# Optimization experiments

Hardware: AMD Instinct MI355X
Metric: run time of the kernel (lower is better)

The kernel has to match this reference:

```python
import jax, jax.numpy as jnp
import numpy as np

B, U, P = 32, 64, 8          # dialogues, utterances per dialogue, parties per dialogue
V, D, L = 32000, 300, 256    # vocab, emb_dim, sentence length
H, S = 5, 5                  # n_heads, n_steps
NP = 200                     # global number of parties
MAXLEN = 252
NT = B * (U + P)             # total nodes in batched graph


def setup_inputs() -> dict:
    key = jax.random.key(0)
    ks = iter(jax.random.split(key, 48))
    rn = lambda shape, s=0.02: jax.random.normal(next(ks), shape, jnp.float32) * s
    x = jax.random.randint(next(ks), (B * U, L), 0, V, dtype=jnp.int32)
    ps_local = np.array(jax.random.randint(next(ks), (B, U), 0, P, dtype=jnp.int32))
    # build batched dialogue graph (sequential utterance chain + utterance<->party edges)
    src, dst = [], []
    for g in range(B):
        off = g * (U + P)
        for i in range(U - 1):
            src += [off + i, off + i + 1]; dst += [off + i + 1, off + i]
        for i in range(U):
            q = off + U + int(ps_local[g, i])
            src += [off + i, q]; dst += [q, off + i]
    src = jnp.asarray(np.array(src, np.int32)); dst = jnp.asarray(np.array(dst, np.int32))
    node_ids = np.arange(NT).reshape(B, U + P)
    u_idx = jnp.asarray(node_ids[:, :U].reshape(-1).astype(np.int32))
    q_idx = jnp.asarray(node_ids[:, U:].reshape(-1).astype(np.int32))
    lid = jnp.tile(jnp.arange(U, dtype=jnp.int32), B)
    pids = jax.random.randint(next(ks), (B * P,), 0, NP, dtype=jnp.int32)
    py = jax.random.normal(next(ks), (B,), jnp.float32)
    return dict(
        x=x, src=src, dst=dst, u_idx=u_idx, q_idx=q_idx, lid=lid, pids=pids, py=py,
        word_W=rn((V, D), 1.0),
        conv_w3=rn((100, 1, 3, D)), conv_b3=rn((100,)),
        conv_w4=rn((100, 1, 4, D)), conv_b4=rn((100,)),
        conv_w5=rn((100, 1, 5, D)), conv_b5=rn((100,)),
        party_W=rn((NP, D), 1.0), pos_W=rn((MAXLEN, D)),
        gat_fc=rn((S, D, H * D)), gat_al=rn((S, H, D)), gat_ar=rn((S, H, D)),
        gat_res=rn((S, D, H * D)), gat_b=rn((S, H * D)),
        pa_W=rn((D, D)), pa_b=rn((D,)), pa_c=rn((D,)),
        sa_W=rn((D, D)), sa_b=rn((D,)), sa_c=rn((D,)),
        v_W=rn((1, D)), v_b=rn((D,)),
        out_W=rn((3 * D, 1)), out_b=rn((1,)))


def _text_cnn(emb, cw, cb):
    # emb [N,1,L,D], cw [100,1,w,D] -> valid conv [N,100,L-w+1,1] -> global max pool
    y = jax.lax.conv_general_dilated(emb, cw, (1, 1), 'VALID',
                                     dimension_numbers=('NCHW', 'OIHW', 'NCHW'))
    y = y + cb[None, :, None, None]
    return jnp.max(y, axis=(2, 3))  # [N,100]


def _ctx_attn(xb, W, b, c):
    # xb [B,K,D]; ContextAttention(batch=False) applied per dialogue: softmax over K
    h = jnp.tanh(xb @ W + b)
    a = jax.nn.softmax(h @ c, axis=1)          # [B,K]
    return jnp.einsum('bk,bkd->bd', a, xb)


def reference(x, src, dst, u_idx, q_idx, lid, pids, py,
              word_W, conv_w3, conv_b3, conv_w4, conv_b4, conv_w5, conv_b5,
              party_W, pos_W, gat_fc, gat_al, gat_ar, gat_res, gat_b,
              pa_W, pa_b, pa_c, sa_W, sa_b, sa_c, v_W, v_b, out_W, out_b):
    # text CNN utterance embedding
    emb = word_W[x][:, None, :, :]                       # [Nu,1,L,D]
    wx = jnp.concatenate([_text_cnn(emb, conv_w3, conv_b3),
                          _text_cnn(emb, conv_w4, conv_b4),
                          _text_cnn(emb, conv_w5, conv_b5)], axis=1)  # [Nu,300]
    # node features: utterances (+ positional), parties from party embedding
    feat = jnp.zeros((NT, D), wx.dtype)
    feat = feat.at[u_idx].set(wx + pos_W[lid])
    feat = feat.at[q_idx].set(party_W[pids])
    # n_steps GATConv layers (DGL semantics, residual + bias), mean over heads
    h = feat
    for i in range(S):
        z = (h @ gat_fc[i]).reshape(NT, H, D)            # [NT,H,D]
        el = jnp.einsum('nhd,hd->nh', z, gat_al[i])
        er = jnp.einsum('nhd,hd->nh', z, gat_ar[i])
        e = jax.nn.leaky_relu(el[src] + er[dst], 0.2)    # [E,H]
        m = jax.ops.segment_max(e, dst, num_segments=NT)
        ee = jnp.exp(e - m[dst])
        den = jax.ops.segment_sum(ee, dst, num_segments=NT)
        alpha = ee / den[dst]                            # edge softmax per dst
        agg = jax.ops.segment_sum(alpha[:, :, None] * z[src], dst, num_segments=NT)
        out = agg + (h @ gat_res[i]).reshape(NT, H, D) + gat_b[i].reshape(H, D)
        h = jnp.mean(out, axis=1)                        # [NT,D] (dropout is identity in eval)
    # per-dialogue context-attention pooling over party / sentence nodes
    hu = h[u_idx].reshape(B, U, D)
    hq = h[q_idx].reshape(B, P, D)
    px = _ctx_attn(hq, pa_W, pa_b, pa_c)
    sx = _ctx_attn(hu, sa_W, sa_b, sa_c)
    ox = jnp.concatenate([px, sx, py[:, None] @ v_W + v_b], axis=-1)  # [B,900]
    return ox @ out_W + out_b                            # [B,1]
```

## Files before the change

### kernel.cpp

```cpp
#include <hip/hip_runtime.h>
#include <stdint.h>

#define NUTT 2048
#define NNODE 2304
#define NE 8128

typedef __attribute__((ext_vector_type(8))) short short8;
typedef __attribute__((ext_vector_type(16))) float float16;

__device__ __forceinline__ float16 MFMA(short8 a, short8 b, float16 c) {
  return __builtin_amdgcn_mfma_f32_32x32x16_bf16(a, b, c, 0, 0, 0);
}

__device__ __forceinline__ unsigned short f2b(float f) {
  unsigned int u = __builtin_bit_cast(unsigned int, f);
  u = (u + 0x7FFFu + ((u >> 16) & 1u)) >> 16;
  return (unsigned short)u;
}
__device__ __forceinline__ float b2f(unsigned short h) {
  unsigned int u = ((unsigned int)h) << 16;
  return __builtin_bit_cast(float, u);
}

#define OFF_WW   0u
#define OFF_BCNN 19200000u
#define OFF_BGAT 20183040u
#define OFF_BSA  29521920u
#define OFF_BPA  29716480u
#define OFF_WX   29911040u
#define OFF_H16  32368640u
#define OFF_Z    33806336u
#define OFF_EL   47962112u
#define OFF_ER   48008192u
#define OFF_CNT  48054272u
#define OFF_CUR  48063488u
#define OFF_PTR  48072704u
#define OFF_EID  48082176u

__global__ void pack_wordW(const float* __restrict__ src, unsigned short* __restrict__ dst) {
  int i4 = (blockIdx.x * 256 + threadIdx.x) * 4;
  if (i4 >= 9600000) return;
  const float4 v = *(const float4*)(src + i4);
  uint2 o;
  o.x = (unsigned int)f2b(v.x) | ((unsigned int)f2b(v.y) << 16);
  o.y = (unsigned int)f2b(v.z) | ((unsigned int)f2b(v.w) << 16);
  *(uint2*)(dst + i4) = o;
}

__global__ void pack_cnnB(const float* __restrict__ w3, const float* __restrict__ w4,
                          const float* __restrict__ w5, unsigned short* __restrict__ out) {
  int i = blockIdx.x * 256 + threadIdx.x;
  if (i >= 466944) return;
  int width, local; const float* cw;
  if (i < 116736)      { width = 3; local = i;          cw = w3; }
  else if (i < 272384) { width = 4; local = i - 116736; cw = w4; }
  else                 { width = 5; local = i - 272384; cw = w5; }
  int KS = 19 * width;
  int per_nt = KS * 512;
  int nt = local / per_nt;
  int rem = local - nt * per_nt;
  int ks = rem >> 9;
  int lr = rem & 511;
  int lane = lr >> 3, j = lr & 7;
  int col = nt * 32 + (lane & 31);
  int k = ks * 16 + 8 * (lane >> 5) + j;
  int tap = k / 304, koff = k - tap * 304;
  float v = 0.f;
  if (col < 100 && koff < 300) v = cw[(col * width + tap) * 300 + koff];
  out[i] = f2b(v);
}

__global__ void pack_gatB(const float* __restrict__ fc, const float* __restrict__ res,
                          unsigned short* __restrict__ out) {
  int i = blockIdx.x * 256 + threadIdx.x;
  if (i >= 4669440) return;
  int layer = i / 933888;
  int rem = i - layer * 933888;
  int nt = rem / (19 * 512);
  int r2 = rem - nt * (19 * 512);
  int ks = r2 >> 9;
  int lr = r2 & 511;
  int lane = lr >> 3, j = lr & 7;
  int col = nt * 32 + (lane & 31);
  int k = ks * 16 + 8 * (lane >> 5) + j;
  float v = 0.f;
  if (k < 300) {
    if (col < 1500)      v = fc[((size_t)layer * 300 + k) * 1500 + col];
    else if (col < 3000) v = res[((size_t)layer * 300 + k) * 1500 + (col - 1500)];
  }
  out[i] = f2b(v);
}

__global__ void pack_poolB(const float* __restrict__ W, unsigned short* __restrict__ out) {
  int i = blockIdx.x * 256 + threadIdx.x;
  if (i >= 97280) return;
  int nt = i / (19 * 512);
  int r2 = i - nt * (19 * 512);
  int ks = r2 >> 9;
  int lr = r2 & 511;
  int lane = lr >> 3, j = lr & 7;
  int col = nt * 32 + (lane & 31);
  int k = ks * 16 + 8 * (lane >> 5) + j;
  float v = 0.f;
  if (k < 300 && col < 300) v = W[k * 300 + col];
  out[i] = f2b(v);
}

__global__ void csr_zero(int* cnt, int* cur) {
  int i = blockIdx.x * 256 + threadIdx.x;
  if (i < NNODE) { cnt[i] = 0; cur[i] = 0; }
}
__global__ void csr_count(const int* __restrict__ dst, int* cnt) {
  int e = blockIdx.x * 256 + threadIdx.x;
  if (e < NE) atomicAdd(&cnt[dst[e]], 1);
}
__global__ void csr_scan(const int* __restrict__ cnt, int* __restrict__ ptr) {
  __shared__ int part[256];
  __shared__ int loc[NNODE];
  int t = threadIdx.x;
  int s = 0;
  for (int k = 0; k < 9; ++k) { loc[t * 9 + k] = s; s += cnt[t * 9 + k]; }
  part[t] = s;
  __syncthreads();
  for (int off = 1; off < 256; off <<= 1) {
    int add = (t >= off) ? part[t - off] : 0;
    __syncthreads();
    part[t] += add;
    __syncthreads();
  }
  int base = part[t] - s;
  for (int k = 0; k < 9; ++k) ptr[t * 9 + k] = base + loc[t * 9 + k];
  if (t == 255) ptr[NNODE] = part[255];
}
__global__ void csr_scatter(const int* __restrict__ dst, const int* __restrict__ ptr,
                            int* cur, int* __restrict__ eid) {
  int e = blockIdx.x * 256 + threadIdx.x;
  if (e < NE) {
    int d = dst[e];
    int pos = atomicAdd(&cur[d], 1);
    eid[ptr[d] + pos] = e;
  }
}

template<int W, int WSEC>
__device__ __forceinline__ void cnn_section(const char* sm, float* scratch,
    const unsigned short* Bsec, const float* bias, float* wxrow, int tid) {
  const int KS = 19 * W;
  const int PD = 6;
  int lane = tid & 63, wave = tid >> 6;
  int l31 = lane & 31, g = lane >> 5;
  int Mblk = wave >> 1, ntp = wave & 1;
  float16 acc[2][2] = {};
  const char* bbase = (const char*)Bsec + (size_t)(ntp * 2 * KS) * 1024 + lane * 16;
  short8 pb0[PD], pb1[PD];
  #pragma unroll
  for (int p = 0; p < PD; ++p) {
    pb0[p] = *(const short8*)(bbase + (size_t)p * 1024);
    pb1[p] = *(const short8*)(bbase + (size_t)(KS + p) * 1024);
  }
  int rbase = Mblk * 64 + l31;
  #pragma unroll
  for (int j = 0; j < W; ++j) {
    int q0 = rbase + j;       q0 = (q0 > 255 ? 255 : q0) * 624;
    int q1 = rbase + 32 + j;  q1 = (q1 > 255 ? 255 : q1) * 624;
    #pragma unroll
    for (int kl = 0; kl < 19; ++kl) {
      const int ks = j * 19 + kl;
      int kb = kl * 32 + 16 * g;
      short8 a0 = *(const short8*)(sm + q0 + kb);
      short8 a1 = *(const short8*)(sm + q1 + kb);
      short8 b0 = pb0[ks % PD];
      short8 b1 = pb1[ks % PD];
      if (ks + PD < KS) {
        pb0[ks % PD] = *(const short8*)(bbase + (size_t)(ks + PD) * 1024);
        pb1[ks % PD] = *(const short8*)(bbase + (size_t)(KS + ks + PD) * 1024);
      }
      acc[0][0] = MFMA(a0, b0, acc[0][0]);
      acc[0][1] = MFMA(a0, b1, acc[0][1]);
      acc[1][0] = MFMA(a1, b0, acc[1][0]);
      acc[1][1] = MFMA(a1, b1, acc[1][1]);
    }
  }
  float cm0 = -3.0e38f, cm1 = -3.0e38f;
  #pragma unroll
  for (int mi = 0; mi < 2; ++mi) {
    #pragma unroll
    for (int r = 0; r < 16; ++r) {
      int row = Mblk * 64 + mi * 32 + (r & 3) + 8 * (r >> 2) + 4 * g;
      if (row <= 256 - W) {
        float v0 = acc[mi][0][r], v1 = acc[mi][1][r];
        if (v0 > cm0) cm0 = v0;
        if (v1 > cm1) cm1 = v1;
      }
    }
  }
  cm0 = fmaxf(cm0, __shfl_xor(cm0, 32));
  cm1 = fmaxf(cm1, __shfl_xor(cm1, 32));
  if (lane < 32) {
    scratch[wave * 64 + l31]      = cm0;
    scratch[wave * 64 + 32 + l31] = cm1;
  }
  __syncthreads();
  if (tid < 128) {
    int f = tid;
    if (f < 100) {
      int ntp_f = f >> 6, rest = f & 63;
      float v =        scratch[(0 * 2 + ntp_f) * 64 + rest];
      v = fmaxf(v,     scratch[(1 * 2 + ntp_f) * 64 + rest]);
      v = fmaxf(v,     scratch[(2 * 2 + ntp_f) * 64 + rest]);
      v = fmaxf(v,     scratch[(3 * 2 + ntp_f) * 64 + rest]);
      wxrow[WSEC * 100 + f] = v + bias[f];
    }
  }
  __syncthreads();
}

__global__ __launch_bounds__(512, 2) void cnn_kernel(
    const int* __restrict__ x, const unsigned short* __restrict__ wW,
    const unsigned short* __restrict__ Bcnn,
    const float* __restrict__ cb3, const float* __restrict__ cb4, const float* __restrict__ cb5,
    float* __restrict__ wx) {
  extern __shared__ char sm[];
  int n = blockIdx.x, tid = threadIdx.x;
  float* scratch = (float*)(sm + 159744);
  const int* xr = x + n * 256;
  for (int i = tid; i < 19968; i += 512) {
    int r = i / 78, c = i - r * 78;
    uint2 v; v.x = 0u; v.y = 0u;
    if (c < 75) {
      int tok = xr[r];
      v = *(const uint2*)((const char*)wW + (size_t)tok * 600 + c * 8);
    }
    *(uint2*)(sm + r * 624 + c * 8) = v;
  }
  __syncthreads();
  float* wxrow = wx + (size_t)n * 300;
  cnn_section<3, 0>(sm, scratch, Bcnn,           cb3, wxrow, tid);
  cnn_section<4, 1>(sm, scratch, Bcnn + 116736,  cb4, wxrow, tid);
  cnn_section<5, 2>(sm, scratch, Bcnn + 272384,  cb5, wxrow, tid);
}

__global__ void feat_kernel(const float* __restrict__ wx, const float* __restrict__ posW,
                            const int* __restrict__ lid, const float* __restrict__ partyW,
                            const int* __restrict__ pids, const int* __restrict__ u_idx,
                            const int* __restrict__ q_idx, unsigned short* __restrict__ h16) {
  int b = blockIdx.x, t = threadIdx.x;
  int node = (b < NUTT) ? u_idx[b] : q_idx[b - NUTT];
  for (int d = t; d < 312; d += 64) {
    float v = 0.f;
    if (d < 300)
      v = (b < NUTT) ? (wx[(size_t)b * 300 + d] + posW[(size_t)lid[b] * 300 + d])
                     : partyW[(size_t)pids[b - NUTT] * 300 + d];
    h16[(size_t)node * 312 + d] = (d < 300) ? f2b(v) : (unsigned short)0;
  }
}

__global__ __launch_bounds__(512, 2) void gat_mm(
    const unsigned short* __restrict__ h16, const unsigned short* __restrict__ Bg,
    unsigned short* __restrict__ z) {
  extern __shared__ char sm[];
  int tid = threadIdx.x, lane = tid & 63, wave = tid >> 6;
  int WGm = blockIdx.x, WGn = blockIdx.y;
  const char* srcp = (const char*)h16 + (size_t)WGm * 79872;
  for (int i = tid; i < 4992; i += 512)
    *(uint4*)(sm + i * 16) = *(const uint4*)(srcp + (size_t)i * 16);
  __syncthreads();
  int l31 = lane & 31, g = lane >> 5;
  int Mblk = wave >> 2, Nblk = wave & 3;
  float16 acc[2][2] = {};
  const char* a0 = sm + (Mblk * 64 + l31) * 624 + 16 * g;
  const char* a1 = a0 + 32 * 624;
  const char* b0 = (const char*)Bg + (size_t)((WGn * 8 + Nblk * 2) * 19) * 1024 + lane * 16;
  const char* b1 = b0 + 19 * 1024;
  #pragma unroll 2
  for (int ks = 0; ks < 19; ++ks) {
    short8 A0 = *(const short8*)(a0 + ks * 32);
    short8 A1 = *(const short8*)(a1 + ks * 32);
    short8 B0 = *(const short8*)(b0 + (size_t)ks * 1024);
    short8 B1 = *(const short8*)(b1 + (size_t)ks * 1024);
    acc[0][0] = MFMA(A0, B0, acc[0][0]);
    acc[0][1] = MFMA(A0, B1, acc[0][1]);
    acc[1][0] = MFMA(A1, B0, acc[1][0]);
    acc[1][1] = MFMA(A1, B1, acc[1][1]);
  }
  #pragma unroll
  for (int mi = 0; mi < 2; ++mi)
    #pragma unroll
    for (int ni = 0; ni < 2; ++ni)
      #pragma unroll
      for (int r = 0; r < 16; ++r) {
        int row = WGm * 128 + Mblk * 64 + mi * 32 + (r & 3) + 8 * (r >> 2) + 4 * g;
        int col = WGn * 256 + (Nblk * 2 + ni) * 32 + l31;
        z[(size_t)row * 3072 + col] = f2b(acc[mi][ni][r]);
      }
}

__global__ void gat_edge1(const unsigned short* __restrict__ z,
                          const float* __restrict__ al, const float* __restrict__ ar,
                          float* __restrict__ el, float* __restrict__ er) {
  int node = blockIdx.x * 4 + (threadIdx.x >> 6);
  if (node >= NNODE) return;
  int lane = threadIdx.x & 63;
  for (int h = 0; h < 5; ++h) {
    float accl = 0.f, accr = 0.f;
    for (int d = lane; d < 300; d += 64) {
      float zv = b2f(z[(size_t)node * 3072 + h * 300 + d]);
      accl += zv * al[h * 300 + d];
      accr += zv * ar[h * 300 + d];
    }
    for (int s = 32; s; s >>= 1) {
      accl += __shfl_xor(accl, s);
      accr += __shfl_xor(accr, s);
    }
    if (lane == 0) { el[node * 5 + h] = accl; er[node * 5 + h] = accr; }
  }
}

__global__ __launch_bounds__(320) void gat_edge2(
    const unsigned short* __restrict__ z, const float* __restrict__ el,
    const float* __restrict__ er, const float* __restrict__ gb,
    const int* __restrict__ ptr, const int* __restrict__ eidl,
    const int* __restrict__ srcA, unsigned short* __restrict__ h16out) {
  int dstn = blockIdx.x;
  int tid = threadIdx.x, h = tid >> 6, lane = tid & 63;
  __shared__ float lds5[5][304];
  int p0 = ptr[dstn], deg = ptr[dstn + 1] - p0;
  float ee = 0.f, den = 0.f;
  int sj = 0;
  if (deg > 0) {
    float s = -3.0e38f;
    if (lane < deg) {
      int e = eidl[p0 + lane];
      sj = srcA[e];
      float sv = el[sj * 5 + h] + er[dstn * 5 + h];
      s = (sv >= 0.f) ? sv : 0.2f * sv;
    }
    float m = s;
    for (int t = 32; t; t >>= 1) m = fmaxf(m, __shfl_xor(m, t));
    ee = (lane < deg) ? __expf(s - m) : 0.f;
    den = ee;
    for (int t = 32; t; t >>= 1) den += __shfl_xor(den, t);
  }
  for (int it = 0; it < 5; ++it) {
    int d = lane + it * 64;
    float acc = 0.f;
    if (deg > 0) {
      for (int e = 0; e < deg; ++e) {
        float w = __shfl(ee, e);
        int srow = __shfl(sj, e);
        if (d < 300) acc += w * b2f(z[(size_t)srow * 3072 + h * 300 + d]);
      }
      acc /= den;
    }
    if (d < 300) {
      float res = b2f(z[(size_t)dstn * 3072 + 1500 + h * 300 + d]);
      lds5[h][d] = acc + res + gb[h * 300 + d];
    }
  }
  __syncthreads();
  if (tid < 312) {
    float v = 0.f;
    if (tid < 300)
      v = 0.2f * (lds5[0][tid] + lds5[1][tid] + lds5[2][tid] + lds5[3][tid] + lds5[4][tid]);
    h16out[(size_t)dstn * 312 + tid] = (tid < 300) ? f2b(v) : (unsigned short)0;
  }
}

__device__ __forceinline__ void ctx_attn(const char* XB, int mtiles, int Kvalid,
    const unsigned short* Bw, const float* bias, const float* cvec,
    float* T, float* AA, float* OUT, int tid) {
  int lane = tid & 63, wave = tid >> 6;
  int l31 = lane & 31, g = lane >> 5;
  int ntasks = mtiles * 10;
  for (int t = wave; t < ntasks; t += 8) {
    int nt, mt;
    if (mtiles == 2) { nt = t >> 1; mt = t & 1; } else { nt = t; mt = 0; }
    float16 acc = {};
    const char* ap = XB + (mt * 32 + l31) * 624 + 16 * g;
    const char* bp = (const char*)Bw + (size_t)(nt * 19) * 1024 + lane * 16;
    for (int ks = 0; ks < 19; ++ks) {
      short8 A = *(const short8*)(ap + ks * 32);
      short8 Bv = *(const short8*)(bp + (size_t)ks * 1024);
      acc = MFMA(A, Bv, acc);
    }
    int col = nt * 32 + l31;
    if (col < 300) {
      float bc = bias[col];
      #pragma unroll
      for (int r = 0; r < 16; ++r) {
        int row = mt * 32 + (r & 3) + 8 * (r >> 2) + 4 * g;
        T[row * 305 + col] = tanhf(acc[r] + bc);
      }
    }
  }
  __syncthreads();
  if (tid < 64) {
    float lg = -3.0e38f;
    if (tid < Kvalid) {
      lg = 0.f;
      for (int d = 0; d < 300; ++d) lg += T[tid * 305 + d] * cvec[d];
    }
    AA[tid] = lg;
  }
  __syncthreads();
  if (wave == 0) {
    float v = AA[lane];
    float m = v;
    for (int s2 = 32; s2; s2 >>= 1) m = fmaxf(m, __shfl_xor(m, s2));
    float e = (lane < Kvalid) ? __expf(v - m) : 0.f;
    float s = e;
    for (int s2 = 32; s2; s2 >>= 1) s += __shfl_xor(s, s2);
    AA[lane] = e / s;
  }
  __syncthreads();
  if (tid < 300) {
    float acc = 0.f;
    for (int k = 0; k < Kvalid; ++k)
      acc += AA[k] * b2f(*(const unsigned short*)(XB + k * 624 + tid * 2));
    OUT[tid] = acc;
  }
  __syncthreads();
}

__global__ __launch_bounds__(512) void pool_kernel(
    const unsigned short* __restrict__ h16,
    const int* __restrict__ u_idx, const int* __restrict__ q_idx,
    const float* __restrict__ py,
    const unsigned short* __restrict__ Bsa, const unsigned short* __restrict__ Bpa,
    const float* __restrict__ sab, const float* __restrict__ sac,
    const float* __restrict__ pab, const float* __restrict__ pac,
    const float* __restrict__ vW, const float* __restrict__ vb,
    const float* __restrict__ outW, const float* __restrict__ outb,
    float* __restrict__ dout) {
  extern __shared__ char sm[];
  int b = blockIdx.x, tid = threadIdx.x;
  char* HU = sm;
  char* HQ = sm + 39936;
  float* T   = (float*)(sm + 59904);
  float* AA  = (float*)(sm + 137984);
  float* PX  = (float*)(sm + 138240);
  float* SX  = (float*)(sm + 139456);
  float* RED = (float*)(sm + 140672);
  for (int i = tid; i < 64 * 78; i += 512) {
    int r = i / 78, c = i - r * 78;
    int node = u_idx[b * 64 + r];
    *(uint2*)(HU + r * 624 + c * 8) =
        *(const uint2*)((const char*)h16 + (size_t)node * 624 + c * 8);
  }
  for (int i = tid; i < 32 * 78; i += 512) {
    int r = i / 78, c = i - r * 78;
    uint2 v; v.x = 0u; v.y = 0u;
    if (r < 8) {
      int node = q_idx[b * 8 + r];
      v = *(const uint2*)((const char*)h16 + (size_t)node * 624 + c * 8);
    }
    *(uint2*)(HQ + r * 624 + c * 8) = v;
  }
  __syncthreads();
  ctx_attn(HU, 2, 64, Bsa, sab, sac, T, AA, SX, tid);
  ctx_attn(HQ, 1, 8,  Bpa, pab, pac, T, AA, PX, tid);
  float contrib = 0.f;
  if (tid < 300) {
    float pv = py[b] * vW[tid] + vb[tid];
    contrib = PX[tid] * outW[tid] + SX[tid] * outW[300 + tid] + pv * outW[600 + tid];
  }
  RED[tid] = contrib;
  __syncthreads();
  for (int s = 256; s > 0; s >>= 1) {
    if (tid < s) RED[tid] += RED[tid + s];
    __syncthreads();
  }
  if (tid == 0) dout[b] = RED[0] + outb[0];
}

extern "C" void kernel_launch(void* const* d_in, const int* in_sizes, int n_in,
                              void* d_out, int out_size, void* d_ws, size_t ws_size,
                              hipStream_t stream) {
  (void)in_sizes; (void)n_in; (void)out_size; (void)ws_size;
  const int*   x       = (const int*)d_in[0];
  const int*   srcA    = (const int*)d_in[1];
  const int*   dstA    = (const int*)d_in[2];
  const int*   u_idx   = (const int*)d_in[3];
  const int*   q_idx   = (const int*)d_in[4];
  const int*   lid     = (const int*)d_in[5];
  const int*   pids    = (const int*)d_in[6];
  const float* py      = (const float*)d_in[7];
  const float* word_W  = (const float*)d_in[8];
  const float* cw3     = (const float*)d_in[9];
  const float* cb3     = (const float*)d_in[10];
  const float* cw4     = (const float*)d_in[11];
  const float* cb4     = (const float*)d_in[12];
  const float* cw5     = (const float*)d_in[13];
  const float* cb5     = (const float*)d_in[14];
  const float* party_W = (const float*)d_in[15];
  const float* pos_W   = (const float*)d_in[16];
  const float* gat_fc  = (const float*)d_in[17];
  const float* gat_al  = (const float*)d_in[18];
  const float* gat_ar  = (const float*)d_in[19];
  const float* gat_res = (const float*)d_in[20];
  const float* gat_b   = (const float*)d_in[21];
  const float* pa_W    = (const float*)d_in[22];
  const float* pa_b    = (const float*)d_in[23];
  const float* pa_c    = (const float*)d_in[24];
  const float* sa_W    = (const float*)d_in[25];
  const float* sa_b    = (const float*)d_in[26];
  const float* sa_c    = (const float*)d_in[27];
  const float* v_W     = (const float*)d_in[28];
  const float* v_b     = (const float*)d_in[29];
  const float* out_W   = (const float*)d_in[30];
  const float* out_b   = (const float*)d_in[31];

  char* ws = (char*)d_ws;
  unsigned short* wW16 = (unsigned short*)(ws + OFF_WW);
  unsigned short* Bcnn = (unsigned short*)(ws + OFF_BCNN);
  unsigned short* Bgat = (unsigned short*)(ws + OFF_BGAT);
  unsigned short* Bsa  = (unsigned short*)(ws + OFF_BSA);
  unsigned short* Bpa  = (unsigned short*)(ws + OFF_BPA);
  float*          wx   = (float*)(ws + OFF_WX);
  unsigned short* h16  = (unsigned short*)(ws + OFF_H16);
  unsigned short* z    = (unsigned short*)(ws + OFF_Z);
  float*          el   = (float*)(ws + OFF_EL);
  float*          er   = (float*)(ws + OFF_ER);
  int*            cnt  = (int*)(ws + OFF_CNT);
  int*            cur  = (int*)(ws + OFF_CUR);
  int*            ptr  = (int*)(ws + OFF_PTR);
  int*            eid  = (int*)(ws + OFF_EID);

  (void)hipFuncSetAttribute((const void*)cnn_kernel,
      hipFuncAttributeMaxDynamicSharedMemorySize, 161792);
  (void)hipFuncSetAttribute((const void*)gat_mm,
      hipFuncAttributeMaxDynamicSharedMemorySize, 79872);
  (void)hipFuncSetAttribute((const void*)pool_kernel,
      hipFuncAttributeMaxDynamicSharedMemorySize, 142720);

  pack_wordW<<<dim3(9375), dim3(256), 0, stream>>>(word_W, wW16);
  pack_cnnB<<<dim3(1824), dim3(256), 0, stream>>>(cw3, cw4, cw5, Bcnn);
  pack_gatB<<<dim3(18240), dim3(256), 0, stream>>>(gat_fc, gat_res, Bgat);
  pack_poolB<<<dim3(380), dim3(256), 0, stream>>>(sa_W, Bsa);
  pack_poolB<<<dim3(380), dim3(256), 0, stream>>>(pa_W, Bpa);

  csr_zero<<<dim3(9), dim3(256), 0, stream>>>(cnt, cur);
  csr_count<<<dim3(32), dim3(256), 0, stream>>>(dstA, cnt);
  csr_scan<<<dim3(1), dim3(256), 0, stream>>>(cnt, ptr);
  csr_scatter<<<dim3(32), dim3(256), 0, stream>>>(dstA, ptr, cur, eid);

  cnn_kernel<<<dim3(2048), dim3(512), 161792, stream>>>(x, wW16, Bcnn, cb3, cb4, cb5, wx);
  feat_kernel<<<dim3(NNODE), dim3(64), 0, stream>>>(wx, pos_W, lid, party_W, pids,
                                                    u_idx, q_idx, h16);
  for (int l = 0; l < 5; ++l) {
    gat_mm<<<dim3(18, 12), dim3(512), 79872, stream>>>(h16, Bgat + (size_t)l * 933888, z);
    gat_edge1<<<dim3(576), dim3(256), 0, stream>>>(z, gat_al + l * 1500, gat_ar + l * 1500,
                                                   el, er);
    gat_edge2<<<dim3(NNODE), dim3(320), 0, stream>>>(z, el, er, gat_b + l * 1500,
                                                     ptr, eid, srcA, h16);
  }
  pool_kernel<<<dim3(32), dim3(512), 142720, stream>>>(
      h16, u_idx, q_idx, py, Bsa, Bpa, sa_b, sa_c, pa_b, pa_c,
      v_W, v_b, out_W, out_b, (float*)d_out);
}
```

Measured before the change: 1.137 ms.

## Merge pack and CSR kernels, fuse feat into CNN, precompute attention vectors

Combines all weight-packing launches into one mega kernel and the four CSR-build launches into a single 1024-thread block. The feature-assembly step is folded into the CNN epilogue, so positional embeddings are added there and bf16 rows are written straight into h16, with a small separate kernel handling party nodes. Attention logits are now computed from h using precomputed fc·al / fc·ar vectors instead of reading z back. This cuts launches and z traffic, but the CSR build becomes serial on a single block and the scores are computed from bf16 h rather than from z.

After: 1.131 ms. About the same (-0.5%).

```diff
diff --git a/kernel.cpp b/kernel.cpp
--- a/kernel.cpp
+++ b/kernel.cpp
@@ -27,7 +27,7 @@
 #define OFF_BGAT 20183040u
 #define OFF_BSA  29521920u
 #define OFF_BPA  29716480u
-#define OFF_WX   29911040u
+#define OFF_AV   29911040u
 #define OFF_H16  32368640u
 #define OFF_Z    33806336u
 #define OFF_EL   47962112u
@@ -37,62 +37,8 @@
 #define OFF_PTR  48072704u
 #define OFF_EID  48082176u
 
-__global__ void pack_wordW(const float* __restrict__ src, unsigned short* __restrict__ dst) {
-  int i4 = (blockIdx.x * 256 + threadIdx.x) * 4;
-  if (i4 >= 9600000) return;
-  const float4 v = *(const float4*)(src + i4);
-  uint2 o;
-  o.x = (unsigned int)f2b(v.x) | ((unsigned int)f2b(v.y) << 16);
-  o.y = (unsigned int)f2b(v.z) | ((unsigned int)f2b(v.w) << 16);
-  *(uint2*)(dst + i4) = o;
-}
-
-__global__ void pack_cnnB(const float* __restrict__ w3, const float* __restrict__ w4,
-                          const float* __restrict__ w5, unsigned short* __restrict__ out) {
-  int i = blockIdx.x * 256 + threadIdx.x;
-  if (i >= 466944) return;
-  int width, local; const float* cw;
-  if (i < 116736)      { width = 3; local = i;          cw = w3; }
-  else if (i < 272384) { width = 4; local = i - 116736; cw = w4; }
-  else                 { width = 5; local = i - 272384; cw = w5; }
-  int KS = 19 * width;
-  int per_nt = KS * 512;
-  int nt = local / per_nt;
-  int rem = local - nt * per_nt;
-  int ks = rem >> 9;
-  int lr = rem & 511;
-  int lane = lr >> 3, j = lr & 7;
-  int col = nt * 32 + (lane & 31);
-  int k = ks * 16 + 8 * (lane >> 5) + j;
-  int tap = k / 304, koff = k - tap * 304;
-  float v = 0.f;
-  if (col < 100 && koff < 300) v = cw[(col * width + tap) * 300 + koff];
-  out[i] = f2b(v);
-}
-
-__global__ void pack_gatB(const float* __restrict__ fc, const float* __restrict__ res,
-                          unsigned short* __restrict__ out) {
-  int i = blockIdx.x * 256 + threadIdx.x;
-  if (i >= 4669440) return;
-  int layer = i / 933888;
-  int rem = i - layer * 933888;
-  int nt = rem / (19 * 512);
-  int r2 = rem - nt * (19 * 512);
-  int ks = r2 >> 9;
-  int lr = r2 & 511;
-  int lane = lr >> 3, j = lr & 7;
-  int col = nt * 32 + (lane & 31);
-  int k = ks * 16 + 8 * (lane >> 5) + j;
-  float v = 0.f;
-  if (k < 300) {
-    if (col < 1500)      v = fc[((size_t)layer * 300 + k) * 1500 + col];
-    else if (col < 3000) v = res[((size_t)layer * 300 + k) * 1500 + (col - 1500)];
-  }
-  out[i] = f2b(v);
-}
-
-__global__ void pack_poolB(const float* __restrict__ W, unsigned short* __restrict__ out) {
-  int i = blockIdx.x * 256 + threadIdx.x;
+__device__ __forceinline__ void pool_pack_body(const float* __restrict__ W,
+    unsigned short* __restrict__ out, int i) {
   if (i >= 97280) return;
   int nt = i / (19 * 512);
   int r2 = i - nt * (19 * 512);
@@ -106,36 +52,111 @@
   out[i] = f2b(v);
 }
 
-__global__ void csr_zero(int* cnt, int* cur) {
-  int i = blockIdx.x * 256 + threadIdx.x;
-  if (i < NNODE) { cnt[i] = 0; cur[i] = 0; }
-}
-__global__ void csr_count(const int* __restrict__ dst, int* cnt) {
-  int e = blockIdx.x * 256 + threadIdx.x;
-  if (e < NE) atomicAdd(&cnt[dst[e]], 1);
-}
-__global__ void csr_scan(const int* __restrict__ cnt, int* __restrict__ ptr) {
+__global__ void mega_pack(
+    const float* __restrict__ word_W,
+    const float* __restrict__ w3, const float* __restrict__ w4, const float* __restrict__ w5,
+    const float* __restrict__ fc, const float* __restrict__ res,
+    const float* __restrict__ al, const float* __restrict__ ar,
+    const float* __restrict__ sa_W, const float* __restrict__ pa_W,
+    unsigned short* __restrict__ wW16, unsigned short* __restrict__ Bcnn,
+    unsigned short* __restrict__ Bgat, unsigned short* __restrict__ Bsa,
+    unsigned short* __restrict__ Bpa, float* __restrict__ av) {
+  int blk = blockIdx.x, tid = threadIdx.x;
+  if (blk < 9375) {
+    int i4 = (blk * 256 + tid) * 4;
+    if (i4 >= 9600000) return;
+    const float4 v = *(const float4*)(word_W + i4);
+    uint2 o;
+    o.x = (unsigned int)f2b(v.x) | ((unsigned int)f2b(v.y) << 16);
+    o.y = (unsigned int)f2b(v.z) | ((unsigned int)f2b(v.w) << 16);
+    *(uint2*)(wW16 + i4) = o;
+  } else if (blk < 11199) {
+    int i = (blk - 9375) * 256 + tid;
+    if (i >= 466944) return;
+    int width, local; const float* cw;
+    if (i < 116736)      { width = 3; local = i;          cw = w3; }
+    else if (i < 272384) { width = 4; local = i - 116736; cw = w4; }
+    else                 { width = 5; local = i - 272384; cw = w5; }
+    int KS = 19 * width;
+    int per_nt = KS * 512;
+    int nt = local / per_nt;
+    int rem = local - nt * per_nt;
+    int ks = rem >> 9;
+    int lr = rem & 511;
+    int lane = lr >> 3, j = lr & 7;
+    int col = nt * 32 + (lane & 31);
+    int k = ks * 16 + 8 * (lane >> 5) + j;
+    int tap = k / 304, koff = k - tap * 304;
+    float v = 0.f;
+    if (col < 100 && koff < 300) v = cw[(col * width + tap) * 300 + koff];
+    Bcnn[i] = f2b(v);
+  } else if (blk < 29439) {
+    int i = (blk - 11199) * 256 + tid;
+    if (i >= 4669440) return;
+    int layer = i / 933888;
+    int rem = i - layer * 933888;
+    int nt = rem / (19 * 512);
+    int r2 = rem - nt * (19 * 512);
+    int ks = r2 >> 9;
+    int lr = r2 & 511;
+    int lane = lr >> 3, j = lr & 7;
+    int col = nt * 32 + (lane & 31);
+    int k = ks * 16 + 8 * (lane >> 5) + j;
+    float v = 0.f;
+    if (k < 300) {
+      if (col < 1500)      v = fc[((size_t)layer * 300 + k) * 1500 + col];
+      else if (col < 3000) v = res[((size_t)layer * 300 + k) * 1500 + (col - 1500)];
+    }
+    Bgat[i] = f2b(v);
+  } else if (blk < 29819) {
+    pool_pack_body(sa_W, Bsa, (blk - 29439) * 256 + tid);
+  } else if (blk < 30199) {
+    pool_pack_body(pa_W, Bpa, (blk - 29819) * 256 + tid);
+  } else {
+    int i = (blk - 30199) * 256 + tid;
+    if (i >= 15000) return;
+    int l = i / 3000;
+    int r = i - l * 3000;
+    int k = r / 10, o = r - k * 10;
+    int h = (o < 5) ? o : (o - 5);
+    const float* src = (o < 5) ? al : ar;
+    const float* fr = fc + ((size_t)l * 300 + k) * 1500 + h * 300;
+    const float* sr = src + (size_t)l * 1500 + h * 300;
+    float acc = 0.f;
+    for (int d = 0; d < 300; ++d) acc += fr[d] * sr[d];
+    av[i] = acc;
+  }
+}
+
+__global__ __launch_bounds__(1024) void csr_build(
+    const int* __restrict__ dst, int* __restrict__ cnt, int* __restrict__ cur,
+    int* __restrict__ ptr, int* __restrict__ eid) {
   __shared__ int part[256];
   __shared__ int loc[NNODE];
   int t = threadIdx.x;
+  for (int i = t; i < NNODE; i += 1024) { cnt[i] = 0; cur[i] = 0; }
+  __syncthreads();
+  for (int e = t; e < NE; e += 1024) atomicAdd(&cnt[dst[e]], 1);
+  __syncthreads();
   int s = 0;
-  for (int k = 0; k < 9; ++k) { loc[t * 9 + k] = s; s += cnt[t * 9 + k]; }
-  part[t] = s;
+  if (t < 256) {
+    for (int k = 0; k < 9; ++k) { loc[t * 9 + k] = s; s += cnt[t * 9 + k]; }
+    part[t] = s;
+  }
   __syncthreads();
   for (int off = 1; off < 256; off <<= 1) {
-    int add = (t >= off) ? part[t - off] : 0;
+    int add = (t < 256 && t >= off) ? part[t - off] : 0;
     __syncthreads();
-    part[t] += add;
+    if (t < 256) part[t] += add;
     __syncthreads();
   }
-  int base = part[t] - s;
-  for (int k = 0; k < 9; ++k) ptr[t * 9 + k] = base + loc[t * 9 + k];
-  if (t == 255) ptr[NNODE] = part[255];
-}
-__global__ void csr_scatter(const int* __restrict__ dst, const int* __restrict__ ptr,
-                            int* cur, int* __restrict__ eid) {
-  int e = blockIdx.x * 256 + threadIdx.x;
-  if (e < NE) {
+  if (t < 256) {
+    int base = part[t] - s;
+    for (int k = 0; k < 9; ++k) ptr[t * 9 + k] = base + loc[t * 9 + k];
+    if (t == 255) ptr[NNODE] = part[255];
+  }
+  __syncthreads();
+  for (int e = t; e < NE; e += 1024) {
     int d = dst[e];
     int pos = atomicAdd(&cur[d], 1);
     eid[ptr[d] + pos] = e;
@@ -144,7 +165,8 @@
 
 template<int W, int WSEC>
 __device__ __forceinline__ void cnn_section(const char* sm, float* scratch,
-    const unsigned short* Bsec, const float* bias, float* wxrow, int tid) {
+    const unsigned short* Bsec, const float* bias, const float* posrow,
+    unsigned short* hrow, int tid) {
   const int KS = 19 * W;
   const int PD = 6;
   int lane = tid & 63, wave = tid >> 6;
@@ -159,13 +181,13 @@
     pb1[p] = *(const short8*)(bbase + (size_t)(KS + p) * 1024);
   }
   int rbase = Mblk * 64 + l31;
+  int ks = 0;
   #pragma unroll
   for (int j = 0; j < W; ++j) {
     int q0 = rbase + j;       q0 = (q0 > 255 ? 255 : q0) * 624;
     int q1 = rbase + 32 + j;  q1 = (q1 > 255 ? 255 : q1) * 624;
     #pragma unroll
     for (int kl = 0; kl < 19; ++kl) {
-      const int ks = j * 19 + kl;
       int kb = kl * 32 + 16 * g;
       short8 a0 = *(const short8*)(sm + q0 + kb);
       short8 a1 = *(const short8*)(sm + q1 + kb);
@@ -175,6 +197,7 @@
         pb0[ks % PD] = *(const short8*)(bbase + (size_t)(ks + PD) * 1024);
         pb1[ks % PD] = *(const short8*)(bbase + (size_t)(KS + ks + PD) * 1024);
       }
+      ++ks;
       acc[0][0] = MFMA(a0, b0, acc[0][0]);
       acc[0][1] = MFMA(a0, b1, acc[0][1]);
       acc[1][0] = MFMA(a1, b0, acc[1][0]);
@@ -209,7 +232,8 @@
       v = fmaxf(v,     scratch[(1 * 2 + ntp_f) * 64 + rest]);
       v = fmaxf(v,     scratch[(2 * 2 + ntp_f) * 64 + rest]);
       v = fmaxf(v,     scratch[(3 * 2 + ntp_f) * 64 + rest]);
-      wxrow[WSEC * 100 + f] = v + bias[f];
+      int d = WSEC * 100 + f;
+      hrow[d] = f2b(v + bias[f] + posrow[d]);
     }
   }
   __syncthreads();
@@ -219,7 +243,8 @@
     const int* __restrict__ x, const unsigned short* __restrict__ wW,
     const unsigned short* __restrict__ Bcnn,
     const float* __restrict__ cb3, const float* __restrict__ cb4, const float* __restrict__ cb5,
-    float* __restrict__ wx) {
+    const int* __restrict__ u_idx, const int* __restrict__ lid,
+    const float* __restrict__ posW, unsigned short* __restrict__ h16) {
   extern __shared__ char sm[];
   int n = blockIdx.x, tid = threadIdx.x;
   float* scratch = (float*)(sm + 159744);
@@ -234,25 +259,22 @@
     *(uint2*)(sm + r * 624 + c * 8) = v;
   }
   __syncthreads();
-  float* wxrow = wx + (size_t)n * 300;
-  cnn_section<3, 0>(sm, scratch, Bcnn,           cb3, wxrow, tid);
-  cnn_section<4, 1>(sm, scratch, Bcnn + 116736,  cb4, wxrow, tid);
-  cnn_section<5, 2>(sm, scratch, Bcnn + 272384,  cb5, wxrow, tid);
-}
-
-__global__ void feat_kernel(const float* __restrict__ wx, const float* __restrict__ posW,
-                            const int* __restrict__ lid, const float* __restrict__ partyW,
-                            const int* __restrict__ pids, const int* __restrict__ u_idx,
-                            const int* __restrict__ q_idx, unsigned short* __restrict__ h16) {
+  unsigned short* hrow = h16 + (size_t)u_idx[n] * 312;
+  const float* posrow = posW + (size_t)lid[n] * 300;
+  cnn_section<3, 0>(sm, scratch, Bcnn,           cb3, posrow, hrow, tid);
+  cnn_section<4, 1>(sm, scratch, Bcnn + 116736,  cb4, posrow, hrow, tid);
+  cnn_section<5, 2>(sm, scratch, Bcnn + 272384,  cb5, posrow, hrow, tid);
+  if (tid < 12) hrow[300 + tid] = 0;
+}
+
+__global__ void party_kernel(const float* __restrict__ partyW,
+                             const int* __restrict__ pids, const int* __restrict__ q_idx,
+                             unsigned short* __restrict__ h16) {
   int b = blockIdx.x, t = threadIdx.x;
-  int node = (b < NUTT) ? u_idx[b] : q_idx[b - NUTT];
-  for (int d = t; d < 312; d += 64) {
-    float v = 0.f;
-    if (d < 300)
-      v = (b < NUTT) ? (wx[(size_t)b * 300 + d] + posW[(size_t)lid[b] * 300 + d])
-                     : partyW[(size_t)pids[b - NUTT] * 300 + d];
-    h16[(size_t)node * 312 + d] = (d < 300) ? f2b(v) : (unsigned short)0;
-  }
+  int node = q_idx[b];
+  for (int d = t; d < 312; d += 64)
+    h16[(size_t)node * 312 + d] =
+        (d < 300) ? f2b(partyW[(size_t)pids[b] * 300 + d]) : (unsigned short)0;
 }
 
 __global__ __launch_bounds__(512, 2) void gat_mm(
@@ -295,24 +317,30 @@
       }
 }
 
-__global__ void gat_edge1(const unsigned short* __restrict__ z,
-                          const float* __restrict__ al, const float* __restrict__ ar,
+__global__ void gat_score(const unsigned short* __restrict__ h16,
+                          const float* __restrict__ av,
                           float* __restrict__ el, float* __restrict__ er) {
   int node = blockIdx.x * 4 + (threadIdx.x >> 6);
   if (node >= NNODE) return;
   int lane = threadIdx.x & 63;
-  for (int h = 0; h < 5; ++h) {
-    float accl = 0.f, accr = 0.f;
-    for (int d = lane; d < 300; d += 64) {
-      float zv = b2f(z[(size_t)node * 3072 + h * 300 + d]);
-      accl += zv * al[h * 300 + d];
-      accr += zv * ar[h * 300 + d];
-    }
-    for (int s = 32; s; s >>= 1) {
-      accl += __shfl_xor(accl, s);
-      accr += __shfl_xor(accr, s);
-    }
-    if (lane == 0) { el[node * 5 + h] = accl; er[node * 5 + h] = accr; }
+  float acc[10] = {};
+  for (int c = 0; c < 5; ++c) {
+    int k = c * 64 + lane;
+    if (k < 300) {
+      float hv = b2f(h16[(size_t)node * 312 + k]);
+      const float* ap = av + k * 10;
+      #pragma unroll
+      for (int o = 0; o < 10; ++o) acc[o] += hv * ap[o];
+    }
+  }
+  #pragma unroll
+  for (int o = 0; o < 10; ++o)
+    for (int s = 32; s; s >>= 1) acc[o] += __shfl_xor(acc[o], s);
+  if (lane == 0) {
+    for (int h = 0; h < 5; ++h) {
+      el[node * 5 + h] = acc[h];
+      er[node * 5 + h] = acc[5 + h];
+    }
   }
 }
 
@@ -516,7 +544,7 @@
   unsigned short* Bgat = (unsigned short*)(ws + OFF_BGAT);
   unsigned short* Bsa  = (unsigned short*)(ws + OFF_BSA);
   unsigned short* Bpa  = (unsigned short*)(ws + OFF_BPA);
-  float*          wx   = (float*)(ws + OFF_WX);
+  float*          av   = (float*)(ws + OFF_AV);
   unsigned short* h16  = (unsigned short*)(ws + OFF_H16);
   unsigned short* z    = (unsigned short*)(ws + OFF_Z);
   float*          el   = (float*)(ws + OFF_EL);
@@ -533,24 +561,18 @@
   (void)hipFuncSetAttribute((const void*)pool_kernel,
       hipFuncAttributeMaxDynamicSharedMemorySize, 142720);
 
-  pack_wordW<<<dim3(9375), dim3(256), 0, stream>>>(word_W, wW16);
-  pack_cnnB<<<dim3(1824), dim3(256), 0, stream>>>(cw3, cw4, cw5, Bcnn);
-  pack_gatB<<<dim3(18240), dim3(256), 0, stream>>>(gat_fc, gat_res, Bgat);
-  pack_poolB<<<dim3(380), dim3(256), 0, stream>>>(sa_W, Bsa);
-  pack_poolB<<<dim3(380), dim3(256), 0, stream>>>(pa_W, Bpa);
-
-  csr_zero<<<dim3(9), dim3(256), 0, stream>>>(cnt, cur);
-  csr_count<<<dim3(32), dim3(256), 0, stream>>>(dstA, cnt);
-  csr_scan<<<dim3(1), dim3(256), 0, stream>>>(cnt, ptr);
-  csr_scatter<<<dim3(32), dim3(256), 0, stream>>>(dstA, ptr, cur, eid);
-
-  cnn_kernel<<<dim3(2048), dim3(512), 161792, stream>>>(x, wW16, Bcnn, cb3, cb4, cb5, wx);
-  feat_kernel<<<dim3(NNODE), dim3(64), 0, stream>>>(wx, pos_W, lid, party_W, pids,
-                                                    u_idx, q_idx, h16);
+  mega_pack<<<dim3(30258), dim3(256), 0, stream>>>(
+      word_W, cw3, cw4, cw5, gat_fc, gat_res, gat_al, gat_ar, sa_W, pa_W,
+      wW16, Bcnn, Bgat, Bsa, Bpa, av);
+  csr_build<<<dim3(1), dim3(1024), 0, stream>>>(dstA, cnt, cur, ptr, eid);
+
+  cnn_kernel<<<dim3(2048), dim3(512), 161792, stream>>>(
+      x, wW16, Bcnn, cb3, cb4, cb5, u_idx, lid, pos_W, h16);
+  party_kernel<<<dim3(256), dim3(64), 0, stream>>>(party_W, pids, q_idx, h16);
+
   for (int l = 0; l < 5; ++l) {
     gat_mm<<<dim3(18, 12), dim3(512), 79872, stream>>>(h16, Bgat + (size_t)l * 933888, z);
-    gat_edge1<<<dim3(576), dim3(256), 0, stream>>>(z, gat_al + l * 1500, gat_ar + l * 1500,
-                                                   el, er);
+    gat_score<<<dim3(576), dim3(256), 0, stream>>>(h16, av + l * 3000, el, er);
     gat_edge2<<<dim3(NNODE), dim3(320), 0, stream>>>(z, el, er, gat_b + l * 1500,
                                                      ptr, eid, srcA, h16);
   }
```
